# Performance work log

Measured on AMD Instinct MI355X. Metric: run time of the kernel, lower is better.

Reference implementation:

```python
import jax, jax.numpy as jnp
import numpy as np

SIGMA = 16
P = 2 * SIGMA + 1  # 33x33 patch
OUT = 128          # feature_extractor.output_size
DN = ('NCHW', 'OIHW', 'NCHW')


def setup_inputs() -> dict:
    key = jax.random.key(0)
    ks = jax.random.split(key, 10)
    B, K, H, W = 4, 64, 256, 256
    images_ground = jax.random.normal(ks[0], (B, 3, H, W), jnp.float32)
    images_satellite = jax.random.normal(ks[1], (B, 3, H, W), jnp.float32)
    # normalized keypoints kept in interior so sigma-window crops stay in-bounds
    keypoints_ground = 0.2 + 0.6 * jax.random.uniform(ks[2], (B, K, 2), jnp.float32)
    keypoints_satellite = 0.2 + 0.6 * jax.random.uniform(ks[3], (B, K, 2), jnp.float32)
    # small CNN feature extractor params (conv 3->32 s1, conv 32->64 s2, GAP, linear 64->OUT)
    w1 = jax.random.normal(ks[4], (32, 3, 3, 3), jnp.float32) * 0.1
    b1 = jnp.zeros((32,), jnp.float32)
    w2 = jax.random.normal(ks[5], (64, 32, 3, 3), jnp.float32) * 0.05
    b2 = jnp.zeros((64,), jnp.float32)
    wl = jax.random.normal(ks[6], (OUT, 64), jnp.float32) * 0.1
    bl = jnp.zeros((OUT,), jnp.float32)
    return dict(images_ground=images_ground, images_satellite=images_satellite,
                keypoints_ground=keypoints_ground, keypoints_satellite=keypoints_satellite,
                w1=w1, b1=b1, w2=w2, b2=b2, wl=wl, bl=bl, num_samples=K)


def _cnn(x, w1, b1, w2, b2, wl, bl):
    # x: [M, 3, P, P] -> [M, OUT]
    h = jax.lax.conv_general_dilated(x, w1, (1, 1), 'VALID', dimension_numbers=DN)
    h = jax.nn.relu(h + b1[None, :, None, None])
    h = jax.lax.conv_general_dilated(h, w2, (2, 2), 'VALID', dimension_numbers=DN)
    h = jax.nn.relu(h + b2[None, :, None, None])
    h = h.mean(axis=(2, 3))  # global average pool -> [M, 64]
    return h @ wl.T + bl


def _crop_all(images, kps_px):
    # images: [B,3,H,W]; kps_px: [N,2] pixel (x, y) coords -> patches [N,B,3,P,P]
    B = images.shape[0]
    hw = images.shape[-1]
    starts = jnp.clip(jnp.floor(kps_px).astype(jnp.int32) - SIGMA, 0, hw - P)
    def one(st):
        return jax.lax.dynamic_slice(images, (0, 0, st[1], st[0]), (B, 3, P, P))
    return jax.vmap(one)(starts)


def reference(images_ground, images_satellite, keypoints_ground, keypoints_satellite,
              w1, b1, w2, b2, wl, bl, num_samples):
    kg = (keypoints_ground * images_ground.shape[-1]).reshape(-1, 2)   # [N,2]
    ksat = (keypoints_satellite * images_satellite.shape[-1]).reshape(-1, 2)
    pg = _crop_all(images_ground, kg)        # [N,B,3,P,P]
    ps = _crop_all(images_satellite, ksat)   # [N,B,3,P,P]
    N, B = pg.shape[0], pg.shape[1]
    fg = _cnn(pg.reshape(N * B, 3, P, P), w1, b1, w2, b2, wl, bl)
    fs = _cnn(ps.reshape(N * B, 3, P, P), w1, b1, w2, b2, wl, bl)
    fg = fg.reshape(N, B, OUT).transpose(1, 0, 2)  # features_ground [B,N,OUT]
    fs = fs.reshape(N, B, OUT).transpose(1, 0, 2)
    return jnp.mean((fg - fs) ** 2)
```

## Files before the change

### kernel.cpp

```cpp
#include <hip/hip_runtime.h>

#define HW   256
#define Pp   33
#define PPAD 36
#define OUTF 128
#define SIG  16

#define KCP   40
#define PLROW (2 * 16 * KCP)
#define PLSZ  (8 * PLROW)
#define IMS   40

#define WS_W1FH 0
#define WS_W1FL 512
#define WS_BHI  1024
#define WS_BLO  10240
#define WS_WLT  19456

typedef __attribute__((ext_vector_type(8))) short v8s;
typedef __attribute__((ext_vector_type(4))) float f32x4;

__device__ __forceinline__ unsigned short f2bf_rne(float x) {
  unsigned u = __float_as_uint(x);
  unsigned r = (u + 0x7FFFu + ((u >> 16) & 1u)) >> 16;
  return (unsigned short)r;
}
__device__ __forceinline__ float bf2f(unsigned short h) {
  return __uint_as_float(((unsigned)h) << 16);
}

__global__ __launch_bounds__(256) void prep_kernel(
    const float* __restrict__ w1, const float* __restrict__ w2,
    const float* __restrict__ wl, float* __restrict__ ws,
    float* __restrict__ out) {
  int t = blockIdx.x * 256 + threadIdx.x;
  int stride = gridDim.x * 256;
  if (blockIdx.x == 0 && threadIdx.x == 0) out[0] = 0.0f;
  unsigned short* w1h = (unsigned short*)(ws + WS_W1FH);
  unsigned short* w1lo = (unsigned short*)(ws + WS_W1FL);
  for (int i = t; i < 1024; i += stride) {
    int j  = i & 7;
    int l  = (i >> 3) & 63;
    int nt = i >> 9;
    int k  = 8 * (l >> 4) + j;
    int ch = 16 * nt + (l & 15);
    float v = (k < 27) ? w1[ch * 27 + k] : 0.0f;
    unsigned short h = f2bf_rne(v);
    w1h[i]  = h;
    w1lo[i] = f2bf_rne(v - bf2f(h));
  }
  unsigned short* bhi = (unsigned short*)(ws + WS_BHI);
  unsigned short* blo = (unsigned short*)(ws + WS_BLO);
  for (int i = t; i < 18432; i += stride) {
    int j  = i & 7;
    int l  = (i >> 3) & 63;
    int w  = (i >> 9) & 3;
    int tp = i >> 11;
    int ch = w * 16 + (l & 15);
    int kc = ((l >> 4) << 3) + j;
    int ky = tp / 3, kx = tp - ky * 3;
    float v = w2[ch * 288 + kc * 9 + ky * 3 + kx];
    unsigned short h = f2bf_rne(v);
    bhi[i] = h;
    blo[i] = f2bf_rne(v - bf2f(h));
  }
  for (int i = t; i < 8192; i += stride) {
    int o = i & 127, ii = i >> 7;
    ws[WS_WLT + i] = wl[o * 64 + ii];
  }
}

__global__ __launch_bounds__(256) void patch_cnn_kernel(
    const float* __restrict__ imgG, const float* __restrict__ imgS,
    const float* __restrict__ kpG,  const float* __restrict__ kpS,
    const float* __restrict__ b1g,  const float* __restrict__ b2g,
    const float* __restrict__ blg,  const float* __restrict__ ws,
    float* __restrict__ out) {
  __shared__ __align__(16) unsigned short patch[3 * Pp * PPAD];
  __shared__ __align__(16) unsigned short imcol[4][32 * IMS];
  __shared__ __align__(16) unsigned short hiP[PLSZ];
  __shared__ float gapv[64];
  __shared__ float fstash[OUTF];
  __shared__ float lred[4];

  const int bid  = blockIdx.x;
  const int n    = bid >> 2;
  const int b    = bid & 3;
  const int tid  = threadIdx.x;
  const int wave = tid >> 6;
  const int lane = tid & 63;

  const int m16 = lane & 15;
  const int qq  = lane >> 4;
  const int mt  = wave & 1;
  const int nt  = wave >> 1;

  const int bm = tid & 31;
  const int kq = tid >> 5;
  int  boff[4];
  bool bval[4];
#pragma unroll
  for (int j = 0; j < 4; ++j) {
    int k = 4 * kq + j;
    bval[j] = (k < 27);
    int kk = bval[j] ? k : 0;
    int ci = kk / 9, r2 = kk - ci * 9, ky = r2 / 3, kx = r2 - ky * 3;
    boff[j] = (ci * Pp + ky) * PPAD + bm + kx;
  }

  const v8s w1hF = ((const v8s*)((const unsigned short*)(ws + WS_W1FH)))[nt * 64 + lane];
  const v8s w1lF = ((const v8s*)((const unsigned short*)(ws + WS_W1FL)))[nt * 64 + lane];
  const float b1v = b1g[nt * 16 + m16];

  const v8s* bhW = (const v8s*)((const unsigned short*)(ws + WS_BHI)) + (wave * 64 + lane);
  const v8s* blW = (const v8s*)((const unsigned short*)(ws + WS_BLO)) + (wave * 64 + lane);
  const float b2v = b2g[wave * 16 + m16];

  auto build_row = [&](int r, int ibuf) {
    unsigned short h[4];
#pragma unroll
    for (int j = 0; j < 4; ++j)
      h[j] = bval[j] ? patch[boff[j] + r * PPAD] : (unsigned short)0;
    unsigned w0 = (unsigned)h[0] | ((unsigned)h[1] << 16);
    unsigned w1_ = (unsigned)h[2] | ((unsigned)h[3] << 16);
    *(uint2*)&imcol[ibuf][bm * IMS + 4 * kq] = make_uint2(w0, w1_);
  };

  auto conv1_row = [&](int ibuf, int sl) {
    v8s af = *(const v8s*)&imcol[ibuf][(16 * mt + m16) * IMS + 8 * qq];
    f32x4 a1 = {0.f, 0.f, 0.f, 0.f};
    a1 = __builtin_amdgcn_mfma_f32_16x16x32_bf16(af, w1hF, a1, 0, 0, 0);
    a1 = __builtin_amdgcn_mfma_f32_16x16x32_bf16(af, w1lF, a1, 0, 0, 0);
#pragma unroll
    for (int rg = 0; rg < 4; ++rg) {
      int x = 16 * mt + 4 * qq + rg;
      float f = fmaxf(a1[rg] + b1v, 0.f);
      hiP[((sl * 2 + (x & 1)) * 16 + (x >> 1)) * KCP + 16 * nt + m16] = f2bf_rne(f);
    }
  };

  auto ldA = [&](int sk, int kx) -> v8s {
    const int p = kx & 1;
    int cp = m16 + (kx >> 1); if (cp > 15) cp = 15;
    return *(const v8s*)&hiP[((sk * 2 + p) * 16 + cp) * KCP + qq * 8];
  };

#define TAP2(tp, aA, aB)                                                      \
  { v8s bh_ = bhW[(tp) * 256]; v8s bl_ = blW[(tp) * 256];                     \
    accA = __builtin_amdgcn_mfma_f32_16x16x32_bf16(aA, bh_, accA, 0, 0, 0);   \
    accB = __builtin_amdgcn_mfma_f32_16x16x32_bf16(aB, bh_, accB, 0, 0, 0);   \
    accA = __builtin_amdgcn_mfma_f32_16x16x32_bf16(aA, bl_, accA, 0, 0, 0);   \
    accB = __builtin_amdgcn_mfma_f32_16x16x32_bf16(aB, bl_, accB, 0, 0, 0); }
#define TAP1(tp, aa)                                                          \
  { v8s bh_ = bhW[(tp) * 256]; v8s bl_ = blW[(tp) * 256];                     \
    acc = __builtin_amdgcn_mfma_f32_16x16x32_bf16(aa, bh_, acc, 0, 0, 0);     \
    acc = __builtin_amdgcn_mfma_f32_16x16x32_bf16(aa, bl_, acc, 0, 0, 0); }

  float dd = 0.0f;

#pragma unroll 1
  for (int side = 0; side < 2; ++side) {
    const float* img = side ? imgS : imgG;
    const float* kp  = side ? kpS : kpG;

    int sx = (int)floorf(kp[n * 2 + 0] * 256.0f) - SIG;
    int sy = (int)floorf(kp[n * 2 + 1] * 256.0f) - SIG;
    sx = min(max(sx, 0), HW - Pp);
    sy = min(max(sy, 0), HW - Pp);

    for (int i = tid; i < (3 * Pp * PPAD) / 2; i += 256) {
      int e  = 2 * i;
      int ci = e / (Pp * PPAD);
      int r2 = e - ci * (Pp * PPAD);
      int r  = r2 / PPAD;
      int cc = r2 - r * PPAD;
      float vx = 0.f, vy = 0.f;
      const float* rowp = &img[((b * 3 + ci) * HW + (sy + r)) * HW + sx];
      if (cc < 32) { float2 v = *(const float2*)(rowp + cc); vx = v.x; vy = v.y; }
      else if (cc == 32) { vx = rowp[32]; }
      unsigned pk = (unsigned)f2bf_rne(vx) | ((unsigned)f2bf_rne(vy) << 16);
      *(unsigned*)&patch[e] = pk;
    }
    __syncthreads();
    build_row(0, 0); build_row(1, 1); build_row(2, 2); build_row(3, 3);
    __syncthreads();
    conv1_row(0, 0); conv1_row(1, 1); conv1_row(2, 2); conv1_row(3, 3);
    __syncthreads();
    build_row(4, 0); build_row(5, 1);
    __syncthreads();
    conv1_row(0, 4); conv1_row(1, 5);

    float gapAcc = 0.0f;

#pragma unroll 1
    for (int i = 0; i < 7; ++i) {
      __syncthreads();
      const int s0 = (4 * i)     & 7;
      const int s1 = (4 * i + 1) & 7;
      const int s2 = (4 * i + 2) & 7;
      const int s3 = (4 * i + 3) & 7;
      const int s4 = (4 * i + 4) & 7;
      f32x4 accA = {0.f, 0.f, 0.f, 0.f};
      f32x4 accB = {0.f, 0.f, 0.f, 0.f};
      v8s sh0 = ldA(s2, 0), sh1 = ldA(s2, 1), sh2 = ldA(s2, 2);
      {
        v8s a0 = ldA(s0, 0), a1 = ldA(s0, 1), a2 = ldA(s0, 2);
        TAP2(0, a0, sh0); TAP2(1, a1, sh1); TAP2(2, a2, sh2);
      }
      {
        v8s a0 = ldA(s1, 0), a1 = ldA(s1, 1), a2 = ldA(s1, 2);
        v8s b0 = ldA(s3, 0), b1 = ldA(s3, 1), b2 = ldA(s3, 2);
        TAP2(3, a0, b0); TAP2(4, a1, b1); TAP2(5, a2, b2);
      }
      {
        v8s b0 = ldA(s4, 0), b1 = ldA(s4, 1), b2 = ldA(s4, 2);
        TAP2(6, sh0, b0); TAP2(7, sh1, b1); TAP2(8, sh2, b2);
      }

      const int r0 = 4 * i + 6;
      if (r0     <= 30) build_row(r0,     0);
      if (r0 + 1 <= 30) build_row(r0 + 1, 1);
      if (r0 + 2 <= 30) build_row(r0 + 2, 2);
      if (r0 + 3 <= 30) build_row(r0 + 3, 3);
      __syncthreads();
      if (r0     <= 30) conv1_row(0, r0 & 7);
      if (r0 + 1 <= 30) conv1_row(1, (r0 + 1) & 7);
      if (r0 + 2 <= 30) conv1_row(2, (r0 + 2) & 7);
      if (r0 + 3 <= 30) conv1_row(3, (r0 + 3) & 7);

      {
        float sA = fmaxf(accA.x + b2v, 0.f) + fmaxf(accA.y + b2v, 0.f) +
                   fmaxf(accA.z + b2v, 0.f);
        if (qq < 3) sA += fmaxf(accA.w + b2v, 0.f);
        gapAcc += sA;
        float sB = fmaxf(accB.x + b2v, 0.f) + fmaxf(accB.y + b2v, 0.f) +
                   fmaxf(accB.z + b2v, 0.f);
        if (qq < 3) sB += fmaxf(accB.w + b2v, 0.f);
        gapAcc += sB;
      }
    }

    {
      __syncthreads();
      f32x4 acc = {0.f, 0.f, 0.f, 0.f};
      v8s a0 = ldA(4, 0), a1 = ldA(4, 1), a2 = ldA(4, 2);
      TAP1(0, a0); TAP1(1, a1); TAP1(2, a2);
      v8s c0 = ldA(5, 0), c1 = ldA(5, 1), c2 = ldA(5, 2);
      TAP1(3, c0); TAP1(4, c1); TAP1(5, c2);
      v8s e0 = ldA(6, 0), e1 = ldA(6, 1), e2 = ldA(6, 2);
      TAP1(6, e0); TAP1(7, e1); TAP1(8, e2);
      float s = fmaxf(acc.x + b2v, 0.f) + fmaxf(acc.y + b2v, 0.f) +
                fmaxf(acc.z + b2v, 0.f);
      if (qq < 3) s += fmaxf(acc.w + b2v, 0.f);
      gapAcc += s;
    }

    gapAcc += __shfl_down(gapAcc, 32, 64);
    gapAcc += __shfl_down(gapAcc, 16, 64);
    if (lane < 16) gapv[wave * 16 + m16] = gapAcc * (1.0f / 225.0f);
    __syncthreads();

    if (tid < OUTF) {
      float f = blg[tid];
#pragma unroll 8
      for (int i = 0; i < 64; ++i) f = fmaf(gapv[i], ws[WS_WLT + i * OUTF + tid], f);
      if (side == 0) fstash[tid] = f;
      else { float d = f - fstash[tid]; dd = d * d; }
    }
    __syncthreads();
  }

  dd += __shfl_down(dd, 32, 64);
  dd += __shfl_down(dd, 16, 64);
  dd += __shfl_down(dd, 8, 64);
  dd += __shfl_down(dd, 4, 64);
  dd += __shfl_down(dd, 2, 64);
  dd += __shfl_down(dd, 1, 64);
  if (lane == 0) lred[wave] = dd;
  __syncthreads();
  if (tid == 0) {
    float s = (lred[0] + lred[1]) + (lred[2] + lred[3]);
    atomicAdd(out, s * (1.0f / 131072.0f));
  }
}

extern "C" void kernel_launch(void* const* d_in, const int* in_sizes, int n_in,
                              void* d_out, int out_size, void* d_ws, size_t ws_size,
                              hipStream_t stream) {
  const float* imgG = (const float*)d_in[0];
  const float* imgS = (const float*)d_in[1];
  const float* kpG  = (const float*)d_in[2];
  const float* kpS  = (const float*)d_in[3];
  const float* w1   = (const float*)d_in[4];
  const float* b1   = (const float*)d_in[5];
  const float* w2   = (const float*)d_in[6];
  const float* b2   = (const float*)d_in[7];
  const float* wl   = (const float*)d_in[8];
  const float* bl   = (const float*)d_in[9];
  float* ws  = (float*)d_ws;
  float* out = (float*)d_out;

  hipLaunchKernelGGL(prep_kernel, dim3(32), dim3(256), 0, stream, w1, w2, wl, ws, out);
  hipLaunchKernelGGL(patch_cnn_kernel, dim3(1024), dim3(256), 0, stream,
                     imgG, imgS, kpG, kpS, b1, b2, bl, ws, out);
}
```

Baseline: 149.5 us.

## Compute conv1 rows per-wave directly from patch, removing im2col buffer and barriers

Each wave now builds its conv1 A-fragment straight from the bf16 patch in LDS and computes a full output row (both 16-channel halves), instead of staging an im2col buffer shared across waves. This removes the imcol LDS buffer and the extra __syncthreads per iteration that separated build and conv1 phases. The ring of conv1 rows grows from 8 to 10 slots so the in-loop writes do not overwrite rows still being read, and the last-row A fragments are carried across iterations in registers. The cost is more scattered per-lane LDS reads of patch and more registers for the second set of weights.

New measurement: 143.3 us. 4.1% less time.

```diff
diff --git a/kernel.cpp b/kernel.cpp
--- a/kernel.cpp
+++ b/kernel.cpp
@@ -8,8 +8,8 @@
 
 #define KCP   40
 #define PLROW (2 * 16 * KCP)
-#define PLSZ  (8 * PLROW)
-#define IMS   40
+#define NSLOT 10
+#define PLSZ  (NSLOT * PLROW)
 
 #define WS_W1FH 0
 #define WS_W1FL 512
@@ -77,7 +77,6 @@
     const float* __restrict__ blg,  const float* __restrict__ ws,
     float* __restrict__ out) {
   __shared__ __align__(16) unsigned short patch[3 * Pp * PPAD];
-  __shared__ __align__(16) unsigned short imcol[4][32 * IMS];
   __shared__ __align__(16) unsigned short hiP[PLSZ];
   __shared__ float gapv[64];
   __shared__ float fstash[OUTF];
@@ -92,50 +91,53 @@
 
   const int m16 = lane & 15;
   const int qq  = lane >> 4;
-  const int mt  = wave & 1;
-  const int nt  = wave >> 1;
-
-  const int bm = tid & 31;
-  const int kq = tid >> 5;
-  int  boff[4];
-  bool bval[4];
-#pragma unroll
-  for (int j = 0; j < 4; ++j) {
-    int k = 4 * kq + j;
-    bval[j] = (k < 27);
-    int kk = bval[j] ? k : 0;
+
+  int  koff[8];
+  bool kval[8];
+#pragma unroll
+  for (int j = 0; j < 8; ++j) {
+    int k = 8 * qq + j;
+    kval[j] = (k < 27);
+    int kk = kval[j] ? k : 0;
     int ci = kk / 9, r2 = kk - ci * 9, ky = r2 / 3, kx = r2 - ky * 3;
-    boff[j] = (ci * Pp + ky) * PPAD + bm + kx;
-  }
-
-  const v8s w1hF = ((const v8s*)((const unsigned short*)(ws + WS_W1FH)))[nt * 64 + lane];
-  const v8s w1lF = ((const v8s*)((const unsigned short*)(ws + WS_W1FL)))[nt * 64 + lane];
-  const float b1v = b1g[nt * 16 + m16];
+    koff[j] = (ci * Pp + ky) * PPAD + kx;
+  }
+
+  const v8s* w1fp = (const v8s*)((const unsigned short*)(ws + WS_W1FH));
+  const v8s* w1lp = (const v8s*)((const unsigned short*)(ws + WS_W1FL));
+  const v8s w1hF0 = w1fp[lane],      w1lF0 = w1lp[lane];
+  const v8s w1hF1 = w1fp[64 + lane], w1lF1 = w1lp[64 + lane];
+  const float b1v0 = b1g[m16];
+  const float b1v1 = b1g[16 + m16];
 
   const v8s* bhW = (const v8s*)((const unsigned short*)(ws + WS_BHI)) + (wave * 64 + lane);
   const v8s* blW = (const v8s*)((const unsigned short*)(ws + WS_BLO)) + (wave * 64 + lane);
   const float b2v = b2g[wave * 16 + m16];
 
-  auto build_row = [&](int r, int ibuf) {
-    unsigned short h[4];
-#pragma unroll
-    for (int j = 0; j < 4; ++j)
-      h[j] = bval[j] ? patch[boff[j] + r * PPAD] : (unsigned short)0;
-    unsigned w0 = (unsigned)h[0] | ((unsigned)h[1] << 16);
-    unsigned w1_ = (unsigned)h[2] | ((unsigned)h[3] << 16);
-    *(uint2*)&imcol[ibuf][bm * IMS + 4 * kq] = make_uint2(w0, w1_);
-  };
-
-  auto conv1_row = [&](int ibuf, int sl) {
-    v8s af = *(const v8s*)&imcol[ibuf][(16 * mt + m16) * IMS + 8 * qq];
-    f32x4 a1 = {0.f, 0.f, 0.f, 0.f};
-    a1 = __builtin_amdgcn_mfma_f32_16x16x32_bf16(af, w1hF, a1, 0, 0, 0);
-    a1 = __builtin_amdgcn_mfma_f32_16x16x32_bf16(af, w1lF, a1, 0, 0, 0);
-#pragma unroll
-    for (int rg = 0; rg < 4; ++rg) {
-      int x = 16 * mt + 4 * qq + rg;
-      float f = fmaxf(a1[rg] + b1v, 0.f);
-      hiP[((sl * 2 + (x & 1)) * 16 + (x >> 1)) * KCP + 16 * nt + m16] = f2bf_rne(f);
+  auto conv1_row_local = [&](int r) {
+    const int sl = r % NSLOT;
+    const int rbase = r * PPAD;
+#pragma unroll
+    for (int mtl = 0; mtl < 2; ++mtl) {
+      v8s af;
+#pragma unroll
+      for (int j = 0; j < 8; ++j) {
+        unsigned short v =
+            kval[j] ? patch[koff[j] + rbase + 16 * mtl + m16] : (unsigned short)0;
+        af[j] = (short)v;
+      }
+      f32x4 z = {0.f, 0.f, 0.f, 0.f};
+      f32x4 t0 = __builtin_amdgcn_mfma_f32_16x16x32_bf16(af, w1hF0, z, 0, 0, 0);
+      t0 = __builtin_amdgcn_mfma_f32_16x16x32_bf16(af, w1lF0, t0, 0, 0, 0);
+      f32x4 t1 = __builtin_amdgcn_mfma_f32_16x16x32_bf16(af, w1hF1, z, 0, 0, 0);
+      t1 = __builtin_amdgcn_mfma_f32_16x16x32_bf16(af, w1lF1, t1, 0, 0, 0);
+#pragma unroll
+      for (int rg = 0; rg < 4; ++rg) {
+        int x = 16 * mtl + 4 * qq + rg;
+        int rowoff = ((sl * 2 + (x & 1)) * 16 + (x >> 1)) * KCP;
+        hiP[rowoff + m16]      = f2bf_rne(fmaxf(t0[rg] + b1v0, 0.f));
+        hiP[rowoff + 16 + m16] = f2bf_rne(fmaxf(t1[rg] + b1v1, 0.f));
+      }
     }
   };
 
@@ -182,51 +184,42 @@
       *(unsigned*)&patch[e] = pk;
     }
     __syncthreads();
-    build_row(0, 0); build_row(1, 1); build_row(2, 2); build_row(3, 3);
-    __syncthreads();
-    conv1_row(0, 0); conv1_row(1, 1); conv1_row(2, 2); conv1_row(3, 3);
-    __syncthreads();
-    build_row(4, 0); build_row(5, 1);
-    __syncthreads();
-    conv1_row(0, 4); conv1_row(1, 5);
+    conv1_row_local(wave);
+    if (wave < 2) conv1_row_local(4 + wave);
 
     float gapAcc = 0.0f;
+    v8s n0, n1, n2;
 
 #pragma unroll 1
     for (int i = 0; i < 7; ++i) {
       __syncthreads();
-      const int s0 = (4 * i)     & 7;
-      const int s1 = (4 * i + 1) & 7;
-      const int s2 = (4 * i + 2) & 7;
-      const int s3 = (4 * i + 3) & 7;
-      const int s4 = (4 * i + 4) & 7;
+      const int base = 4 * i;
+      const int s1 = (base + 1) % NSLOT;
+      const int s2 = (base + 2) % NSLOT;
+      const int s3 = (base + 3) % NSLOT;
+      const int s4 = (base + 4) % NSLOT;
+      if (i == 0) { n0 = ldA(0, 0); n1 = ldA(0, 1); n2 = ldA(0, 2); }
+      const v8s a00 = n0, a01 = n1, a02 = n2;
       f32x4 accA = {0.f, 0.f, 0.f, 0.f};
       f32x4 accB = {0.f, 0.f, 0.f, 0.f};
       v8s sh0 = ldA(s2, 0), sh1 = ldA(s2, 1), sh2 = ldA(s2, 2);
       {
-        v8s a0 = ldA(s0, 0), a1 = ldA(s0, 1), a2 = ldA(s0, 2);
-        TAP2(0, a0, sh0); TAP2(1, a1, sh1); TAP2(2, a2, sh2);
-      }
-      {
-        v8s a0 = ldA(s1, 0), a1 = ldA(s1, 1), a2 = ldA(s1, 2);
-        v8s b0 = ldA(s3, 0), b1 = ldA(s3, 1), b2 = ldA(s3, 2);
-        TAP2(3, a0, b0); TAP2(4, a1, b1); TAP2(5, a2, b2);
-      }
-      {
-        v8s b0 = ldA(s4, 0), b1 = ldA(s4, 1), b2 = ldA(s4, 2);
-        TAP2(6, sh0, b0); TAP2(7, sh1, b1); TAP2(8, sh2, b2);
-      }
-
-      const int r0 = 4 * i + 6;
-      if (r0     <= 30) build_row(r0,     0);
-      if (r0 + 1 <= 30) build_row(r0 + 1, 1);
-      if (r0 + 2 <= 30) build_row(r0 + 2, 2);
-      if (r0 + 3 <= 30) build_row(r0 + 3, 3);
-      __syncthreads();
-      if (r0     <= 30) conv1_row(0, r0 & 7);
-      if (r0 + 1 <= 30) conv1_row(1, (r0 + 1) & 7);
-      if (r0 + 2 <= 30) conv1_row(2, (r0 + 2) & 7);
-      if (r0 + 3 <= 30) conv1_row(3, (r0 + 3) & 7);
+        TAP2(0, a00, sh0); TAP2(1, a01, sh1); TAP2(2, a02, sh2);
+      }
+      {
+        v8s r10 = ldA(s1, 0), r11 = ldA(s1, 1), r12 = ldA(s1, 2);
+        v8s r30 = ldA(s3, 0), r31 = ldA(s3, 1), r32 = ldA(s3, 2);
+        TAP2(3, r10, r30); TAP2(4, r11, r31); TAP2(5, r12, r32);
+      }
+      {
+        n0 = ldA(s4, 0); n1 = ldA(s4, 1); n2 = ldA(s4, 2);
+        TAP2(6, sh0, n0); TAP2(7, sh1, n1); TAP2(8, sh2, n2);
+      }
+
+      {
+        const int r = base + 6 + wave;
+        if (r <= 30) conv1_row_local(r);
+      }
 
       {
         float sA = fmaxf(accA.x + b2v, 0.f) + fmaxf(accA.y + b2v, 0.f) +
@@ -243,11 +236,10 @@
     {
       __syncthreads();
       f32x4 acc = {0.f, 0.f, 0.f, 0.f};
-      v8s a0 = ldA(4, 0), a1 = ldA(4, 1), a2 = ldA(4, 2);
-      TAP1(0, a0); TAP1(1, a1); TAP1(2, a2);
-      v8s c0 = ldA(5, 0), c1 = ldA(5, 1), c2 = ldA(5, 2);
+      TAP1(0, n0); TAP1(1, n1); TAP1(2, n2);
+      v8s c0 = ldA(9, 0), c1 = ldA(9, 1), c2 = ldA(9, 2);
       TAP1(3, c0); TAP1(4, c1); TAP1(5, c2);
-      v8s e0 = ldA(6, 0), e1 = ldA(6, 1), e2 = ldA(6, 2);
+      v8s e0 = ldA(0, 0), e1 = ldA(0, 1), e2 = ldA(0, 2);
       TAP1(6, e0); TAP1(7, e1); TAP1(8, e2);
       float s = fmaxf(acc.x + b2v, 0.f) + fmaxf(acc.y + b2v, 0.f) +
                 fmaxf(acc.z + b2v, 0.f);
```
